# Kernel tuning notes

Measured on AMD Instinct MI355X. Metric: run time of the kernel, lower is better.

Reference implementation:

```python
import jax, jax.numpy as jnp
import numpy as np

B, S, HID, H = 2, 2048, 1024, 16
D = HID // H
LAMBDA_INIT = 0.8
GN_EPS = 1e-5


def setup_inputs() -> dict:
    rng = jax.random.key(0)
    ks = jax.random.split(rng, 12)
    w = 0.02
    return {
        "query": jax.random.normal(ks[0], (B, S, HID), dtype=jnp.float32),
        "key": jax.random.normal(ks[1], (B, S, HID), dtype=jnp.float32),
        "value": jax.random.normal(ks[2], (B, S, HID), dtype=jnp.float32),
        "attention_mask": jnp.ones((B, S), dtype=jnp.float32),
        # params ([in, out] layout; x @ W)
        "Wq": jax.random.normal(ks[3], (HID, H * D * 2), dtype=jnp.float32) * w,
        "Wk": jax.random.normal(ks[4], (HID, H * D * 2), dtype=jnp.float32) * w,
        "Wv": jax.random.normal(ks[5], (HID, H * D), dtype=jnp.float32) * w,
        "Wo": jax.random.normal(ks[6], (H * D, HID), dtype=jnp.float32) * w,
        "lam_q1": jax.random.normal(ks[7], (D,), dtype=jnp.float32),
        "lam_q2": jax.random.normal(ks[8], (D,), dtype=jnp.float32),
        "lam_k1": jax.random.normal(ks[9], (D,), dtype=jnp.float32),
        "lam_k2": jax.random.normal(ks[10], (D,), dtype=jnp.float32),
        "gn_weight": jnp.ones((H * D,), dtype=jnp.float32),
        "gn_bias": jnp.zeros((H * D,), dtype=jnp.float32),
    }


def reference(query, key, value, attention_mask, Wq, Wk, Wv, Wo,
              lam_q1, lam_q2, lam_k1, lam_k2, gn_weight, gn_bias):
    b, s, hid = query.shape
    h, d = H, hid // H
    rs = 1.0 / jnp.sqrt(jnp.asarray(d, query.dtype))

    q = (query @ Wq).reshape(b, s, h, 2 * d).transpose(0, 2, 1, 3)   # [b,h,s,2d]
    k = (key @ Wk).reshape(b, s, h, 2 * d).transpose(0, 2, 1, 3)
    v = (value @ Wv).reshape(b, s, h, d).transpose(0, 2, 1, 3)       # [b,h,s,d]

    Q1, Q2 = q[..., :d], q[..., d:]
    K1, K2 = k[..., :d], k[..., d:]
    s1 = jnp.einsum('bhqd,bhkd->bhqk', Q1, K1) * rs
    s2 = jnp.einsum('bhqd,bhkd->bhqk', Q2, K2) * rs

    # ALiBi bias: slopes[h] * (pos_q - pos_k), subtracted from scores
    pos = jnp.arange(s, dtype=query.dtype)
    slopes = 2.0 ** (-8.0 * jnp.arange(1, h + 1, dtype=query.dtype) / h)
    alibi = slopes[None, :, None, None] * (pos[:, None] - pos[None, :])[None, None]
    causal = jnp.triu(jnp.full((s, s), -1e9, dtype=query.dtype), k=1)[None, None]
    pad = (1.0 - attention_mask)[:, None, None, :] * -1e9
    add = -alibi + causal + pad

    w1 = jax.nn.softmax(s1 + add, axis=-1)
    w2 = jax.nn.softmax(s2 + add, axis=-1)

    lam = (jnp.exp(jnp.dot(lam_q1, lam_k1))
           - jnp.exp(jnp.dot(lam_q2, lam_k2)) + LAMBDA_INIT)
    dw = w1 - lam * w2

    attn = jnp.einsum('bhqk,bhkd->bhqd', dw, v).transpose(0, 2, 1, 3)  # [b,s,h,d]

    # GroupNorm(groups=h, channels=h*d) over [b, C, L]: per (b, head) normalize over (seq, d)
    mean = attn.mean(axis=(1, 3), keepdims=True)
    var = ((attn - mean) ** 2).mean(axis=(1, 3), keepdims=True)
    normed = (attn - mean) / jnp.sqrt(var + GN_EPS)
    normed = normed * gn_weight.reshape(1, 1, h, d) + gn_bias.reshape(1, 1, h, d)

    out = normed * (1.0 - LAMBDA_INIT)
    return out.reshape(b, s, h * d) @ Wo
```

## Files before the change

### kernel.cpp

```cpp
#include <hip/hip_runtime.h>
#include <cstdint>
#include <cstddef>

#define SQ 2048
#define NH 16
#define DH 64
#define HIDN 1024

typedef __attribute__((ext_vector_type(8))) short bf16x8;
typedef __attribute__((ext_vector_type(4))) float f32x4;
typedef __attribute__((ext_vector_type(2))) unsigned u32x2;

__device__ inline short f2b(float x) {
  union { float f; unsigned u; } un; un.f = x;
  unsigned r = un.u + 0x7fffu + ((un.u >> 16) & 1u);
  return (short)(r >> 16);
}

__device__ inline unsigned cvt_pk(float lo, float hi) {
  unsigned r;
  asm("v_cvt_pk_bf16_f32 %0, %1, %2" : "=v"(r) : "v"(lo), "v"(hi));
  return r;
}

__device__ inline f32x4 mfma16(u32x2 a, u32x2 b, f32x4 c) {
  asm("v_mfma_f32_16x16x16_bf16 %0, %1, %2, %0" : "+v"(c) : "v"(a), "v"(b));
  return c;
}

__device__ inline void gl_lds16(const void* g, void* l) {
  __builtin_amdgcn_global_load_lds(
      (const __attribute__((address_space(1))) void*)g,
      (__attribute__((address_space(3))) void*)l, 16, 0, 0);
}

__global__ __launch_bounds__(256) void qkv_to_bf16(const float4* __restrict__ q,
                                                   const float4* __restrict__ k,
                                                   const float4* __restrict__ v,
                                                   short4* __restrict__ out) {
  int i = blockIdx.x * 256 + threadIdx.x;
  const float4* src = (i < 1048576) ? q : ((i < 2097152) ? k : v);
  float4 val = src[i & 1048575];
  short4 o;
  o.x = f2b(val.x); o.y = f2b(val.y); o.z = f2b(val.z); o.w = f2b(val.w);
  out[i] = o;
}

__global__ __launch_bounds__(256) void wconv4(const float* __restrict__ Wq,
                                              const float* __restrict__ Wk,
                                              const float* __restrict__ Wv,
                                              const float* __restrict__ Wo,
                                              short* __restrict__ WqT, short* __restrict__ WkT,
                                              short* __restrict__ WvT, short* __restrict__ WoT) {
  __shared__ float t[32][33];
  int z = blockIdx.z;
  int N = (z < 2) ? 2048 : 1024;
  if (blockIdx.x * 32 >= N) return;
  const float* W = (z == 0) ? Wq : (z == 1) ? Wk : (z == 2) ? Wv : Wo;
  short* Wt = (z == 0) ? WqT : (z == 1) ? WkT : (z == 2) ? WvT : WoT;
  const int K = 1024;
  int n0 = blockIdx.x * 32, k0 = blockIdx.y * 32;
  int tx = threadIdx.x & 31, ty = threadIdx.x >> 5;
#pragma unroll
  for (int r = 0; r < 4; ++r)
    t[ty + r * 8][tx] = W[(size_t)(k0 + ty + r * 8) * N + n0 + tx];
  __syncthreads();
#pragma unroll
  for (int r = 0; r < 4; ++r)
    Wt[(size_t)(n0 + ty + r * 8) * K + k0 + tx] = f2b(t[tx][ty + r * 8]);
}

__global__ void lam_k(const float* __restrict__ q1, const float* __restrict__ q2,
                      const float* __restrict__ k1, const float* __restrict__ k2,
                      float* __restrict__ out) {
  int i = threadIdx.x;
  float d1 = q1[i] * k1[i], d2 = q2[i] * k2[i];
#pragma unroll
  for (int x = 1; x < 64; x <<= 1) { d1 += __shfl_xor(d1, x); d2 += __shfl_xor(d2, x); }
  if (i == 0) out[0] = __expf(d1) - __expf(d2) + 0.8f;
}

__global__ __launch_bounds__(256) void padk(const float* __restrict__ mask,
                                            float* __restrict__ padl2) {
  int i = blockIdx.x * 256 + threadIdx.x;
  padl2[i] = (1.0f - mask[i]) * (-1.0e9f) * 1.44269504089f;
}

__global__ __launch_bounds__(256) void proj3(const short* __restrict__ Abase,
                                             const short* __restrict__ Btbase,
                                             short* __restrict__ QKout,
                                             short* __restrict__ Vtb) {
  const int z = blockIdx.z;
  if (z == 2 && blockIdx.x >= 8) return;
  const int K = 1024;
  const short* A = Abase + (size_t)z * 4194304;
  const short* Bt = Btbase + (size_t)z * 2097152;

  __shared__ __align__(16) short As[128 * 64];
  __shared__ __align__(16) short Bs[128 * 64];
  const int tid = threadIdx.x;
  const int lane = tid & 63, w = tid >> 6;
  const int l15 = lane & 15, lhi = lane >> 4;
  const int wr = w >> 1, wc = w & 1;
  const int m0 = blockIdx.y * 128, n0 = blockIdx.x * 128;

  f32x4 acc[4][4];
#pragma unroll
  for (int i = 0; i < 4; ++i)
#pragma unroll
    for (int j = 0; j < 4; ++j) acc[i][j] = (f32x4){0.f, 0.f, 0.f, 0.f};

  const short* Ag = A + (size_t)m0 * K;
  const short* Bg = Bt + (size_t)n0 * K;

  for (int k0 = 0; k0 < K; k0 += 64) {
#pragma unroll
    for (int it = 0; it < 4; ++it) {
      int idx = it * 256 + tid;
      int row = idx >> 3, c8 = (idx & 7) << 3;
      gl_lds16(Ag + (size_t)row * K + (k0 + c8), &As[idx << 3]);
      gl_lds16(Bg + (size_t)row * K + (k0 + c8), &Bs[idx << 3]);
    }
    __syncthreads();
#pragma unroll
    for (int kk = 0; kk < 64; kk += 32) {
      bf16x8 af[4], bfr[4];
#pragma unroll
      for (int mi = 0; mi < 4; ++mi)
        af[mi] = *(const bf16x8*)&As[(wr * 64 + mi * 16 + l15) * 64 + kk + lhi * 8];
#pragma unroll
      for (int ni = 0; ni < 4; ++ni)
        bfr[ni] = *(const bf16x8*)&Bs[(wc * 64 + ni * 16 + l15) * 64 + kk + lhi * 8];
#pragma unroll
      for (int mi = 0; mi < 4; ++mi)
#pragma unroll
        for (int ni = 0; ni < 4; ++ni)
          acc[mi][ni] = __builtin_amdgcn_mfma_f32_16x16x32_bf16(af[mi], bfr[ni], acc[mi][ni], 0, 0, 0);
    }
    __syncthreads();
  }

#pragma unroll
  for (int mi = 0; mi < 4; ++mi) {
#pragma unroll
    for (int ni = 0; ni < 4; ++ni) {
#pragma unroll
      for (int j = 0; j < 4; ++j) {
        int m = m0 + wr * 64 + mi * 16 + (lhi << 2) + j;
        int n = n0 + wc * 64 + ni * 16 + l15;
        float v = acc[mi][ni][j];
        int s = m & (SQ - 1), bb = m >> 11;
        if (z < 2) {
          int h = n >> 7, t = n & 127, path = t >> 6, tt = t & 63;
          (QKout + (size_t)z * 8388608)
              [((((size_t)(bb * NH + h) * 2 + path) * SQ + s) << 6) + tt] = f2b(v);
        } else {
          int h = n >> 6, t = n & 63;
          Vtb[(((size_t)(bb * NH + h) << 6) + t) * SQ + s] = f2b(v);
        }
      }
    }
  }
}

__global__ __launch_bounds__(256) void gemm_out(const short* __restrict__ A,
                                                const short* __restrict__ Bt,
                                                float* __restrict__ Cout) {
  const int N = 1024, K = 1024;
  __shared__ __align__(16) short As[128 * 64];
  __shared__ __align__(16) short Bs[128 * 64];
  const int tid = threadIdx.x;
  const int lane = tid & 63, w = tid >> 6;
  const int l15 = lane & 15, lhi = lane >> 4;
  const int wr = w >> 1, wc = w & 1;
  const int m0 = blockIdx.y * 128, n0 = blockIdx.x * 128;

  f32x4 acc[4][4];
#pragma unroll
  for (int i = 0; i < 4; ++i)
#pragma unroll
    for (int j = 0; j < 4; ++j) acc[i][j] = (f32x4){0.f, 0.f, 0.f, 0.f};

  const short* Ag = A + (size_t)m0 * K;
  const short* Bg = Bt + (size_t)n0 * K;

  for (int k0 = 0; k0 < K; k0 += 64) {
#pragma unroll
    for (int it = 0; it < 4; ++it) {
      int idx = it * 256 + tid;
      int row = idx >> 3, c8 = (idx & 7) << 3;
      gl_lds16(Ag + (size_t)row * K + (k0 + c8), &As[idx << 3]);
      gl_lds16(Bg + (size_t)row * K + (k0 + c8), &Bs[idx << 3]);
    }
    __syncthreads();
#pragma unroll
    for (int kk = 0; kk < 64; kk += 32) {
      bf16x8 af[4], bfr[4];
#pragma unroll
      for (int mi = 0; mi < 4; ++mi)
        af[mi] = *(const bf16x8*)&As[(wr * 64 + mi * 16 + l15) * 64 + kk + lhi * 8];
#pragma unroll
      for (int ni = 0; ni < 4; ++ni)
        bfr[ni] = *(const bf16x8*)&Bs[(wc * 64 + ni * 16 + l15) * 64 + kk + lhi * 8];
#pragma unroll
      for (int mi = 0; mi < 4; ++mi)
#pragma unroll
        for (int ni = 0; ni < 4; ++ni)
          acc[mi][ni] = __builtin_amdgcn_mfma_f32_16x16x32_bf16(af[mi], bfr[ni], acc[mi][ni], 0, 0, 0);
    }
    __syncthreads();
  }

#pragma unroll
  for (int mi = 0; mi < 4; ++mi)
#pragma unroll
    for (int ni = 0; ni < 4; ++ni)
#pragma unroll
      for (int j = 0; j < 4; ++j) {
        int m = m0 + wr * 64 + mi * 16 + (lhi << 2) + j;
        int n = n0 + wc * 64 + ni * 16 + l15;
        Cout[(size_t)m * N + n] = acc[mi][ni][j];
      }
}

__global__ __launch_bounds__(256) void diff_attn(
    const short* __restrict__ Qp, const short* __restrict__ Kp,
    const short* __restrict__ Vt, const float* __restrict__ padl2,
    const float* __restrict__ lamp, float* __restrict__ attn,
    float* __restrict__ part) {
  __shared__ __align__(16) short K1s[2][64 * 64];
  __shared__ __align__(16) short K2s[2][64 * 64];
  __shared__ __align__(16) short Vts[2][64 * 64];
  __shared__ float red[8];

  const int bid = blockIdx.x;
  const int rk = bid >> 5, bh = bid & 31;
  const int qtA = 31 - rk, qtB = rk;
  const int ntA = qtA + 1, ntT = ntA + qtB + 1;
  const int b = bh >> 4, h = bh & 15;
  const int tid = threadIdx.x, lane = tid & 63, w = tid >> 6;
  const int l15 = lane & 15, lhi = lane >> 4;
  const int sw7 = l15 & 7;
  const int u0 = (lhi ^ sw7) << 3, u1 = ((4 + lhi) ^ sw7) << 3;

  const float L2E = 1.44269504089f;
  const float slope = exp2f(-0.5f * (float)(h + 1));
  const float SC = 0.125f * L2E;
  const float sl2 = slope * L2E;

  f32x4 ck[4];
#pragma unroll
  for (int cf = 0; cf < 4; ++cf)
#pragma unroll
    for (int j = 0; j < 4; ++j)
      ck[cf][j] = sl2 * (float)(16 * cf + 4 * lhi + j);

  const short* Q1g = Qp + (((size_t)bh * 2 + 0) * SQ) * DH;
  const short* Q2g = Qp + (((size_t)bh * 2 + 1) * SQ) * DH;
  const short* K1g = Kp + (((size_t)bh * 2 + 0) * SQ) * DH;
  const short* K2g = Kp + (((size_t)bh * 2 + 1) * SQ) * DH;
  const short* Vtg = Vt + (size_t)bh * DH * SQ;
  const float* padb = padl2 + (b << 11);

  int ucf[4];
#pragma unroll
  for (int cf = 0; cf < 4; ++cf)
    ucf[cf] = (((2 * cf + (lhi >> 1)) ^ sw7) << 1) + (lhi & 1);

  const int sidx0 = tid, sidx1 = 256 + tid;
  const int srow0 = sidx0 >> 3, sus0 = ((sidx0 & 7) ^ (srow0 & 7)) << 3;
  const int srow1 = sidx1 >> 3, sus1 = ((sidx1 & 7) ^ (srow1 & 7)) << 3;

#define STAGE(buf, k0s)                                                          \
  {                                                                              \
    gl_lds16(K1g + (size_t)((k0s) + srow0) * DH + sus0, &K1s[buf][sidx0 << 3]);  \
    gl_lds16(K2g + (size_t)((k0s) + srow0) * DH + sus0, &K2s[buf][sidx0 << 3]);  \
    gl_lds16(Vtg + (size_t)srow0 * SQ + (k0s) + sus0, &Vts[buf][sidx0 << 3]);    \
    gl_lds16(K1g + (size_t)((k0s) + srow1) * DH + sus1, &K1s[buf][sidx1 << 3]);  \
    gl_lds16(K2g + (size_t)((k0s) + srow1) * DH + sus1, &K2s[buf][sidx1 << 3]);  \
    gl_lds16(Vtg + (size_t)srow1 * SQ + (k0s) + sus1, &Vts[buf][sidx1 << 3]);    \
  }

  int cur = 0;
  int itg = 0;
  STAGE(0, 0);
  asm volatile("s_waitcnt vmcnt(0)" ::: "memory");
  __builtin_amdgcn_s_barrier();

  const float lamv = lamp[0];

  for (int ph = 0; ph < 2; ++ph) {
    const int qt = ph ? qtB : qtA;
    const int nt = qt + 1;
    const int wq0 = qt * 64 + (w << 4);
    const int q = wq0 + l15;
    const float qb8 = sl2 * (float)q + 8.0f;

    bf16x8 aq[2][2];
#pragma unroll
    for (int kk = 0; kk < 2; ++kk) {
      aq[0][kk] = *(const bf16x8*)&Q1g[(size_t)q * DH + kk * 32 + lhi * 8];
      aq[1][kk] = *(const bf16x8*)&Q2g[(size_t)q * DH + kk * 32 + lhi * 8];
    }
    f32x4 cq[4];
#pragma unroll
    for (int cf = 0; cf < 4; ++cf)
#pragma unroll
      for (int j = 0; j < 4; ++j) cq[cf][j] = ck[cf][j] - qb8;

    f32x4 acc[2][4];
    float ll[2] = {0.f, 0.f};
#pragma unroll
    for (int p = 0; p < 2; ++p)
#pragma unroll
      for (int i = 0; i < 4; ++i) acc[p][i] = (f32x4){0.f, 0.f, 0.f, 0.f};

    for (int kt = 0; kt < nt; ++kt, ++itg) {
      const int k0 = kt << 6;
      int g = itg + 1;
      if (g < ntT) {
        int k0n = ((g < ntA) ? g : g - ntA) << 6;
        STAGE(cur ^ 1, k0n);
      }

      const float t0 = sl2 * (float)k0;
      f32x4 base4[4];
#pragma unroll
      for (int cf = 0; cf < 4; ++cf) {
        f32x4 p4 = *(const f32x4*)&padb[k0 + 16 * cf + 4 * lhi];
#pragma unroll
        for (int j = 0; j < 4; ++j) base4[cf][j] = cq[cf][j] + (t0 + p4[j]);
      }
      const bool diag = (kt == nt - 1);

      u32x2 pa[2][4];
#pragma unroll
      for (int p = 0; p < 2; ++p) {
        const short* Ks = (p == 0) ? K1s[cur] : K2s[cur];
        f32x4 sv[4];
#pragma unroll
        for (int cf = 0; cf < 4; ++cf) {
          int rb = (cf * 16 + l15) << 6;
          f32x4 z = (f32x4){0.f, 0.f, 0.f, 0.f};
          bf16x8 ka = *(const bf16x8*)&Ks[rb + u0];
          bf16x8 kb = *(const bf16x8*)&Ks[rb + u1];
          sv[cf] = __builtin_amdgcn_mfma_f32_16x16x32_bf16(ka, aq[p][0], z, 0, 0, 0);
          sv[cf] = __builtin_amdgcn_mfma_f32_16x16x32_bf16(kb, aq[p][1], sv[cf], 0, 0, 0);
        }
        float rsum = 0.f;
#pragma unroll
        for (int cf = 0; cf < 4; ++cf) {
          float pv[4];
#pragma unroll
          for (int j = 0; j < 4; ++j) pv[j] = sv[cf][j] * SC + base4[cf][j];
          if (diag) {
#pragma unroll
            for (int j = 0; j < 4; ++j) {
              int kc = k0 + 16 * cf + 4 * lhi + j;
              pv[j] = (kc > q) ? -1.0e9f : pv[j];
            }
          }
          float e0 = exp2f(pv[0]);
          float e1 = exp2f(pv[1]);
          float e2 = exp2f(pv[2]);
          float e3 = exp2f(pv[3]);
          rsum += (e0 + e1) + (e2 + e3);
          pa[p][cf][0] = cvt_pk(e0, e1);
          pa[p][cf][1] = cvt_pk(e2, e3);
        }
        ll[p] += rsum;
      }

#pragma unroll
      for (int df = 0; df < 4; ++df) {
        const u32x2* vrow = (const u32x2*)&Vts[cur][(df * 16 + l15) << 6];
#pragma unroll
        for (int cf = 0; cf < 4; ++cf) {
          u32x2 vb = vrow[ucf[cf]];
          acc[0][df] = mfma16(pa[0][cf], vb, acc[0][df]);
          acc[1][df] = mfma16(pa[1][cf], vb, acc[1][df]);
        }
      }

      asm volatile("s_waitcnt vmcnt(0)" ::: "memory");
      __builtin_amdgcn_s_barrier();
      cur ^= 1;
    }

#pragma unroll
    for (int p = 0; p < 2; ++p) {
      ll[p] += __shfl_xor(ll[p], 16);
      ll[p] += __shfl_xor(ll[p], 32);
    }
    float li1 = 1.0f / ll[0], li2 = lamv / ll[1];
    float li1b[4], li2b[4];
#pragma unroll
    for (int j = 0; j < 4; ++j) {
      li1b[j] = __shfl(li1, (lhi << 2) + j);
      li2b[j] = __shfl(li2, (lhi << 2) + j);
    }
    float lsum = 0.f, lsq = 0.f;
#pragma unroll
    for (int df = 0; df < 4; ++df)
#pragma unroll
      for (int j = 0; j < 4; ++j) {
        int qq = wq0 + (lhi << 2) + j;
        float o = acc[0][df][j] * li1b[j] - acc[1][df][j] * li2b[j];
        attn[((size_t)b * SQ + qq) * HIDN + (h << 6) + (df << 4) + l15] = o;
        lsum += o; lsq += o * o;
      }
#pragma unroll
    for (int x = 1; x < 64; x <<= 1) {
      lsum += __shfl_xor(lsum, x);
      lsq += __shfl_xor(lsq, x);
    }
    if (lane == 0) { red[w] = lsum; red[4 + w] = lsq; }
    __syncthreads();
    if (tid == 0) {
      part[((size_t)bh * 32 + qt) * 2] = red[0] + red[1] + red[2] + red[3];
      part[((size_t)bh * 32 + qt) * 2 + 1] = red[4] + red[5] + red[6] + red[7];
    }
  }
#undef STAGE
}

__global__ void stats_fin(const float* __restrict__ part, float* __restrict__ mi) {
  int bh = threadIdx.x;
  float s = 0.f, ss = 0.f;
  for (int t = 0; t < 32; ++t) {
    s += part[(bh * 32 + t) * 2];
    ss += part[(bh * 32 + t) * 2 + 1];
  }
  float n = (float)(SQ * DH);
  float mean = s / n;
  float var = ss / n - mean * mean;
  mi[bh * 2] = mean;
  mi[bh * 2 + 1] = rsqrtf(var + 1e-5f);
}

__global__ __launch_bounds__(256) void gn_apply(const float* __restrict__ attn,
                                                const float* __restrict__ mi,
                                                const float* __restrict__ gnw,
                                                const float* __restrict__ gnb,
                                                short* __restrict__ X) {
  size_t i = (size_t)blockIdx.x * 256 + threadIdx.x;
  size_t base = i << 2;
  int r = (int)(base >> 10);
  int c = (int)(base & 1023);
  int bh = ((r >> 11) << 4) + (c >> 6);
  float mean = mi[bh * 2], inv = mi[bh * 2 + 1];
  float4 a = *(const float4*)&attn[base];
  short4 o;
  o.x = f2b(((a.x - mean) * inv * gnw[c + 0] + gnb[c + 0]) * 0.2f);
  o.y = f2b(((a.y - mean) * inv * gnw[c + 1] + gnb[c + 1]) * 0.2f);
  o.z = f2b(((a.z - mean) * inv * gnw[c + 2] + gnb[c + 2]) * 0.2f);
  o.w = f2b(((a.w - mean) * inv * gnw[c + 3] + gnb[c + 3]) * 0.2f);
  *(short4*)&X[base] = o;
}

extern "C" void kernel_launch(void* const* d_in, const int* in_sizes, int n_in,
                              void* d_out, int out_size, void* d_ws, size_t ws_size,
                              hipStream_t stream) {
  const float* query = (const float*)d_in[0];
  const float* key = (const float*)d_in[1];
  const float* value = (const float*)d_in[2];
  const float* mask = (const float*)d_in[3];
  const float* Wq = (const float*)d_in[4];
  const float* Wk = (const float*)d_in[5];
  const float* Wv = (const float*)d_in[6];
  const float* Wo = (const float*)d_in[7];
  const float* lq1 = (const float*)d_in[8];
  const float* lq2 = (const float*)d_in[9];
  const float* lk1 = (const float*)d_in[10];
  const float* lk2 = (const float*)d_in[11];
  const float* gnw = (const float*)d_in[12];
  const float* gnb = (const float*)d_in[13];

  char* ws = (char*)d_ws;
  short* WqT = (short*)(ws + 0);
  short* WkT = (short*)(ws + 4194304);
  short* WvT = (short*)(ws + 8388608);
  short* WoT = (short*)(ws + 10485760);
  short* qb = (short*)(ws + 12582912);
  short* Qp = (short*)(ws + 37748736);
  short* Kp = (short*)(ws + 54525952);
  short* Vtb = (short*)(ws + 71303168);
  float* attn = (float*)(ws + 12582912);
  short* X = (short*)(ws + 29360128);
  float* part = (float*)(ws + 79691776);
  float* mi = (float*)(ws + 79708160);
  float* lam = (float*)(ws + 79708416);
  float* padl2 = (float*)(ws + 79708672);

  qkv_to_bf16<<<12288, 256, 0, stream>>>((const float4*)query, (const float4*)key,
                                         (const float4*)value, (short4*)qb);
  wconv4<<<dim3(64, 32, 4), 256, 0, stream>>>(Wq, Wk, Wv, Wo, WqT, WkT, WvT, WoT);
  lam_k<<<1, 64, 0, stream>>>(lq1, lq2, lk1, lk2, lam);
  padk<<<16, 256, 0, stream>>>(mask, padl2);

  proj3<<<dim3(16, 32, 3), 256, 0, stream>>>(qb, WqT, Qp, Vtb);

  diff_attn<<<dim3(512), 256, 0, stream>>>(Qp, Kp, Vtb, padl2, lam, attn, part);
  stats_fin<<<1, 32, 0, stream>>>(part, mi);
  gn_apply<<<4096, 256, 0, stream>>>(attn, mi, gnw, gnb, X);
  gemm_out<<<dim3(8, 32), 256, 0, stream>>>(X, WoT, (float*)d_out);
}
```

Measured before the change: 226.3 us.

## Double-buffer LDS, XOR-swizzle tiles, and remap blocks in projection GEMMs

Both the QKV projection and output GEMMs now stage K-tiles into two LDS buffers, prefetching the next tile while MFMAs run on the current one. Tile columns are XOR-swizzled by row to avoid LDS bank conflicts on fragment reads. The grid is flattened and remapped so consecutive blocks spread across XCDs, and the z==2 early-exit blocks are dropped. The cost is double the LDS footprint, which may lower occupancy, plus a full vmcnt wait before each barrier.

```diff
diff --git a/kernel.cpp b/kernel.cpp
--- a/kernel.cpp
+++ b/kernel.cpp
@@ -86,23 +86,39 @@
   padl2[i] = (1.0f - mask[i]) * (-1.0e9f) * 1.44269504089f;
 }
 
+#define STAGEP(buf, k0s)                                                        \
+  {                                                                             \
+    _Pragma("unroll") for (int it_ = 0; it_ < 4; ++it_) {                       \
+      int idx_ = it_ * 256 + tid;                                               \
+      int row_ = idx_ >> 3, u_ = idx_ & 7;                                      \
+      int us_ = (u_ ^ (row_ & 7)) << 3;                                         \
+      gl_lds16(Ag + (size_t)row_ * 1024 + (k0s) + us_, &As[buf][idx_ << 3]);    \
+      gl_lds16(Bg + (size_t)row_ * 1024 + (k0s) + us_, &Bs[buf][idx_ << 3]);    \
+    }                                                                           \
+  }
+
 __global__ __launch_bounds__(256) void proj3(const short* __restrict__ Abase,
                                              const short* __restrict__ Btbase,
                                              short* __restrict__ QKout,
                                              short* __restrict__ Vtb) {
-  const int z = blockIdx.z;
-  if (z == 2 && blockIdx.x >= 8) return;
-  const int K = 1024;
-  const short* A = Abase + (size_t)z * 4194304;
-  const short* Bt = Btbase + (size_t)z * 2097152;
-
-  __shared__ __align__(16) short As[128 * 64];
-  __shared__ __align__(16) short Bs[128 * 64];
+  __shared__ __align__(16) short As[2][128 * 64];
+  __shared__ __align__(16) short Bs[2][128 * 64];
+  const int bid = blockIdx.x;
+  const int wk = (bid & 7) * 160 + (bid >> 3);
+  int z, my, nx;
+  if (wk < 1024) { z = wk >> 9; int r = wk & 511; my = r >> 4; nx = r & 15; }
+  else { z = 2; int r = wk - 1024; my = r >> 3; nx = r & 7; }
+
   const int tid = threadIdx.x;
   const int lane = tid & 63, w = tid >> 6;
   const int l15 = lane & 15, lhi = lane >> 4;
+  const int sw7 = l15 & 7;
+  const int u0 = (lhi ^ sw7) << 3, u1 = ((4 + lhi) ^ sw7) << 3;
   const int wr = w >> 1, wc = w & 1;
-  const int m0 = blockIdx.y * 128, n0 = blockIdx.x * 128;
+  const int m0 = my * 128, n0 = nx * 128;
+
+  const short* Ag = Abase + (size_t)z * 4194304 + (size_t)m0 * 1024;
+  const short* Bg = Btbase + (size_t)z * 2097152 + (size_t)n0 * 1024;
 
   f32x4 acc[4][4];
 #pragma unroll
@@ -110,34 +126,32 @@
 #pragma unroll
     for (int j = 0; j < 4; ++j) acc[i][j] = (f32x4){0.f, 0.f, 0.f, 0.f};
 
-  const short* Ag = A + (size_t)m0 * K;
-  const short* Bg = Bt + (size_t)n0 * K;
-
-  for (int k0 = 0; k0 < K; k0 += 64) {
-#pragma unroll
-    for (int it = 0; it < 4; ++it) {
-      int idx = it * 256 + tid;
-      int row = idx >> 3, c8 = (idx & 7) << 3;
-      gl_lds16(Ag + (size_t)row * K + (k0 + c8), &As[idx << 3]);
-      gl_lds16(Bg + (size_t)row * K + (k0 + c8), &Bs[idx << 3]);
-    }
-    __syncthreads();
-#pragma unroll
-    for (int kk = 0; kk < 64; kk += 32) {
+  int cur = 0;
+  STAGEP(0, 0);
+  asm volatile("s_waitcnt vmcnt(0)" ::: "memory");
+  __builtin_amdgcn_s_barrier();
+
+  for (int kt = 0; kt < 16; ++kt) {
+    if (kt < 15) STAGEP(cur ^ 1, (kt + 1) * 64);
+#pragma unroll
+    for (int kh = 0; kh < 2; ++kh) {
+      const int uk = kh ? u1 : u0;
       bf16x8 af[4], bfr[4];
 #pragma unroll
       for (int mi = 0; mi < 4; ++mi)
-        af[mi] = *(const bf16x8*)&As[(wr * 64 + mi * 16 + l15) * 64 + kk + lhi * 8];
+        af[mi] = *(const bf16x8*)&As[cur][((wr * 64 + mi * 16 + l15) << 6) + uk];
 #pragma unroll
       for (int ni = 0; ni < 4; ++ni)
-        bfr[ni] = *(const bf16x8*)&Bs[(wc * 64 + ni * 16 + l15) * 64 + kk + lhi * 8];
+        bfr[ni] = *(const bf16x8*)&Bs[cur][((wc * 64 + ni * 16 + l15) << 6) + uk];
 #pragma unroll
       for (int mi = 0; mi < 4; ++mi)
 #pragma unroll
         for (int ni = 0; ni < 4; ++ni)
           acc[mi][ni] = __builtin_amdgcn_mfma_f32_16x16x32_bf16(af[mi], bfr[ni], acc[mi][ni], 0, 0, 0);
     }
-    __syncthreads();
+    asm volatile("s_waitcnt vmcnt(0)" ::: "memory");
+    __builtin_amdgcn_s_barrier();
+    cur ^= 1;
   }
 
 #pragma unroll
@@ -166,14 +180,22 @@
 __global__ __launch_bounds__(256) void gemm_out(const short* __restrict__ A,
                                                 const short* __restrict__ Bt,
                                                 float* __restrict__ Cout) {
-  const int N = 1024, K = 1024;
-  __shared__ __align__(16) short As[128 * 64];
-  __shared__ __align__(16) short Bs[128 * 64];
+  __shared__ __align__(16) short As[2][128 * 64];
+  __shared__ __align__(16) short Bs[2][128 * 64];
+  const int bid = blockIdx.x;
+  const int wk = (bid & 7) * 32 + (bid >> 3);
+  const int my = wk >> 3, nx = wk & 7;
+
   const int tid = threadIdx.x;
   const int lane = tid & 63, w = tid >> 6;
   const int l15 = lane & 15, lhi = lane >> 4;
+  const int sw7 = l15 & 7;
+  const int u0 = (lhi ^ sw7) << 3, u1 = ((4 + lhi) ^ sw7) << 3;
   const int wr = w >> 1, wc = w & 1;
-  const int m0 = blockIdx.y * 128, n0 = blockIdx.x * 128;
+  const int m0 = my * 128, n0 = nx * 128;
+
+  const short* Ag = A + (size_t)m0 * 1024;
+  const short* Bg = Bt + (size_t)n0 * 1024;
 
   f32x4 acc[4][4];
 #pragma unroll
@@ -181,34 +203,32 @@
 #pragma unroll
     for (int j = 0; j < 4; ++j) acc[i][j] = (f32x4){0.f, 0.f, 0.f, 0.f};
 
-  const short* Ag = A + (size_t)m0 * K;
-  const short* Bg = Bt + (size_t)n0 * K;
-
-  for (int k0 = 0; k0 < K; k0 += 64) {
-#pragma unroll
-    for (int it = 0; it < 4; ++it) {
-      int idx = it * 256 + tid;
-      int row = idx >> 3, c8 = (idx & 7) << 3;
-      gl_lds16(Ag + (size_t)row * K + (k0 + c8), &As[idx << 3]);
-      gl_lds16(Bg + (size_t)row * K + (k0 + c8), &Bs[idx << 3]);
-    }
-    __syncthreads();
-#pragma unroll
-    for (int kk = 0; kk < 64; kk += 32) {
+  int cur = 0;
+  STAGEP(0, 0);
+  asm volatile("s_waitcnt vmcnt(0)" ::: "memory");
+  __builtin_amdgcn_s_barrier();
+
+  for (int kt = 0; kt < 16; ++kt) {
+    if (kt < 15) STAGEP(cur ^ 1, (kt + 1) * 64);
+#pragma unroll
+    for (int kh = 0; kh < 2; ++kh) {
+      const int uk = kh ? u1 : u0;
       bf16x8 af[4], bfr[4];
 #pragma unroll
       for (int mi = 0; mi < 4; ++mi)
-        af[mi] = *(const bf16x8*)&As[(wr * 64 + mi * 16 + l15) * 64 + kk + lhi * 8];
+        af[mi] = *(const bf16x8*)&As[cur][((wr * 64 + mi * 16 + l15) << 6) + uk];
 #pragma unroll
       for (int ni = 0; ni < 4; ++ni)
-        bfr[ni] = *(const bf16x8*)&Bs[(wc * 64 + ni * 16 + l15) * 64 + kk + lhi * 8];
+        bfr[ni] = *(const bf16x8*)&Bs[cur][((wc * 64 + ni * 16 + l15) << 6) + uk];
 #pragma unroll
       for (int mi = 0; mi < 4; ++mi)
 #pragma unroll
         for (int ni = 0; ni < 4; ++ni)
           acc[mi][ni] = __builtin_amdgcn_mfma_f32_16x16x32_bf16(af[mi], bfr[ni], acc[mi][ni], 0, 0, 0);
     }
-    __syncthreads();
+    asm volatile("s_waitcnt vmcnt(0)" ::: "memory");
+    __builtin_amdgcn_s_barrier();
+    cur ^= 1;
   }
 
 #pragma unroll
@@ -219,7 +239,7 @@
       for (int j = 0; j < 4; ++j) {
         int m = m0 + wr * 64 + mi * 16 + (lhi << 2) + j;
         int n = n0 + wc * 64 + ni * 16 + l15;
-        Cout[(size_t)m * N + n] = acc[mi][ni][j];
+        Cout[(size_t)m * 1024 + n] = acc[mi][ni][j];
       }
 }
 
@@ -498,10 +518,10 @@
   lam_k<<<1, 64, 0, stream>>>(lq1, lq2, lk1, lk2, lam);
   padk<<<16, 256, 0, stream>>>(mask, padl2);
 
-  proj3<<<dim3(16, 32, 3), 256, 0, stream>>>(qb, WqT, Qp, Vtb);
+  proj3<<<dim3(1280), 256, 0, stream>>>(qb, WqT, Qp, Vtb);
 
   diff_attn<<<dim3(512), 256, 0, stream>>>(Qp, Kp, Vtb, padl2, lam, attn, part);
   stats_fin<<<1, 32, 0, stream>>>(part, mi);
   gn_apply<<<4096, 256, 0, stream>>>(attn, mi, gnw, gnb, X);
-  gemm_out<<<dim3(8, 32), 256, 0, stream>>>(X, WoT, (float*)d_out);
-}
+  gemm_out<<<dim3(256), 256, 0, stream>>>(X, WoT, (float*)d_out);
+}
```

Result: faster. 221.5 us (-2.1%).
